# Kernel tuning notes

Hardware: AMD Instinct MI355X
Metric: run time of the kernel (lower is better)

Reference implementation:

```python
import jax, jax.numpy as jnp
import numpy as np

B = 65536      # batch
C = 1000       # num_classes
D = 256        # feat_dim


def _l2norm(x, eps=1e-12):
    # matches F.normalize(dim=1): v / max(||v||_2, eps)
    n = jnp.linalg.norm(x, axis=1, keepdims=True)
    return x / jnp.maximum(n, eps)


def setup_inputs() -> dict:
    key = jax.random.key(0)
    k1, k2, k3, k4, k5 = jax.random.split(key, 5)
    bound = 1.0 / np.sqrt(D)
    X = jax.random.normal(k1, (B, D), dtype=jnp.float32)
    labels = jax.random.randint(k2, (B,), 0, C)
    signatures = jax.random.uniform(k3, (C, D), dtype=jnp.float32, minval=-bound, maxval=bound)
    b_means = jax.random.uniform(k4, (1, D), dtype=jnp.float32, minval=-bound, maxval=bound)
    b_covs = jax.random.normal(k5, (D, D), dtype=jnp.float32)
    return {"X": X, "labels": labels, "signatures": signatures,
            "b_means": b_means, "b_covs": b_covs}


def reference(X, labels, signatures, b_means, b_covs):
    # SVD-based whitening of background covariance (tiny DxD)
    cov = b_covs @ b_covs.T
    U, eig, _ = jnp.linalg.svd(cov)
    DU = (eig ** -0.5)[:, None] * U.T              # diag(eig^-1/2) @ U^T, [D, D]
    xHat = _l2norm((X - b_means) @ DU.T)           # [B, D]
    sHat = _l2norm(signatures @ DU.T)              # [C, D]
    ACE_targets = xHat @ sHat.T                    # [B, C] cosine scores
    labels = labels.astype(jnp.int32)
    numerator = jnp.take_along_axis(ACE_targets, labels[:, None], axis=1)[:, 0]
    # denominator = exp(true) + sum(exp(others)) == sum over all classes
    loss = -jnp.mean(numerator - jax.nn.logsumexp(ACE_targets, axis=1))
    return (loss, ACE_targets)
```

## Files before the change

### kernel.cpp

```cpp
#include <hip/hip_runtime.h>
#include <hip/hip_bf16.h>
#include <math.h>

#define D_ 256
#define B_ 65536
#define C_ 1000

typedef _Float16 f16x8 __attribute__((ext_vector_type(8)));
typedef float f32x4 __attribute__((ext_vector_type(4)));

__global__ __launch_bounds__(256) void cov_kernel(const float* __restrict__ bc,
                                                  double* __restrict__ C64,
                                                  double* __restrict__ acc,
                                                  unsigned int* __restrict__ counter) {
  __shared__ float Ash[32][260];
  __shared__ float Bsh2[32][260];
  const int b = blockIdx.x, bi = b >> 3, bj = b & 7;
  const int e = threadIdx.x;
  if (b == 0 && e == 0) { *acc = 0.0; *counter = 0u; }
#pragma unroll
  for (int s = 0; s < 32; ++s) {
    int lin = s * 256 + e;
    int rr = lin >> 8, cc = lin & 255;
    Ash[rr][cc] = bc[(bi * 32 + rr) * 256 + cc];
    Bsh2[rr][cc] = bc[(bj * 32 + rr) * 256 + cc];
  }
  __syncthreads();
  const int tx = e & 15, ty = e >> 4;
  double a00 = 0, a01 = 0, a10 = 0, a11 = 0;
#pragma unroll 8
  for (int k = 0; k < 256; ++k) {
    double ar0 = (double)Ash[ty][k], ar1 = (double)Ash[ty + 16][k];
    double br0 = (double)Bsh2[tx][k], br1 = (double)Bsh2[tx + 16][k];
    a00 += ar0 * br0; a01 += ar0 * br1;
    a10 += ar1 * br0; a11 += ar1 * br1;
  }
  const int r0 = bi * 32, c0 = bj * 32;
  C64[(size_t)(r0 + ty) * D_ + c0 + tx] = a00;
  C64[(size_t)(r0 + ty) * D_ + c0 + tx + 16] = a01;
  C64[(size_t)(r0 + ty + 16) * D_ + c0 + tx] = a10;
  C64[(size_t)(r0 + ty + 16) * D_ + c0 + tx + 16] = a11;
}

__global__ __launch_bounds__(256, 1) void chol_panel(double* __restrict__ A, int p) {
  const int j0 = p * 64;
  const int r = threadIdx.x;
  __shared__ double raw[2][64];
  double pr[64];
  const bool act = (r >= j0);
  const bool inpanel = act && (r < j0 + 64);
  if (act) {
#pragma unroll
    for (int k = 0; k < 64; ++k) pr[k] = A[(size_t)r * D_ + j0 + k];
  }
  if (inpanel) raw[0][r - j0] = pr[0];
  __syncthreads();
#pragma unroll
  for (int j = 0; j < 64; ++j) {
    const int col = j0 + j;
    const double d2 = raw[j & 1][j];
    double rs = (double)rsqrtf((float)d2);
    rs = rs * (1.5 - 0.5 * d2 * rs * rs);
    rs = rs * (1.5 - 0.5 * d2 * rs * rs);
    if (r >= col) {
      const double lr_ = pr[j] * rs;
      pr[j] = lr_;
#pragma unroll
      for (int k = j + 1; k < 64; ++k) pr[k] -= lr_ * (raw[j & 1][k] * rs);
    }
    if (j < 63) {
      if (r > col && r < j0 + 64) raw[(j + 1) & 1][r - j0] = pr[j + 1];
    }
    __syncthreads();
  }
  if (act) {
    const int kmax = (r - j0 < 63) ? (r - j0) : 63;
#pragma unroll
    for (int k = 0; k < 64; ++k)
      if (k <= kmax) A[(size_t)r * D_ + j0 + k] = pr[k];
  }
}

__global__ __launch_bounds__(256) void chol_trail(double* __restrict__ A, int p) {
  const int j0 = p * 64;
  const int t0 = j0 + 64;
  int b = blockIdx.x, I = 0;
  while (b >= I + 1) { b -= I + 1; ++I; }
  const int J = b;
  const int r0 = t0 + I * 64, c0 = t0 + J * 64;
  __shared__ double LR[64][67];
  __shared__ double LC[64][67];
  const int tid = threadIdx.x;
  for (int e = tid; e < 64 * 64; e += 256) {
    int rr = e >> 6, cc = e & 63;
    LR[rr][cc] = A[(size_t)(r0 + rr) * D_ + j0 + cc];
    LC[rr][cc] = A[(size_t)(c0 + rr) * D_ + j0 + cc];
  }
  __syncthreads();
  const int tx = tid & 15, ty = tid >> 4;
  double acc[4][4];
#pragma unroll
  for (int i = 0; i < 4; ++i)
#pragma unroll
    for (int j = 0; j < 4; ++j) acc[i][j] = 0.0;
#pragma unroll 4
  for (int k = 0; k < 64; ++k) {
    double a_[4], b_[4];
#pragma unroll
    for (int i = 0; i < 4; ++i) a_[i] = LR[ty + 16 * i][k];
#pragma unroll
    for (int j = 0; j < 4; ++j) b_[j] = LC[tx + 16 * j][k];
#pragma unroll
    for (int i = 0; i < 4; ++i)
#pragma unroll
      for (int j = 0; j < 4; ++j) acc[i][j] += a_[i] * b_[j];
  }
#pragma unroll
  for (int i = 0; i < 4; ++i) {
    const int grow = r0 + ty + 16 * i;
#pragma unroll
    for (int j = 0; j < 4; ++j) {
      const int gcol = c0 + tx + 16 * j;
      A[(size_t)grow * D_ + gcol] -= acc[i][j];
    }
  }
}

__global__ __launch_bounds__(256) void inv_kernel(const double* __restrict__ L,
                                                  _Float16* __restrict__ WbP,
                                                  _Float16* __restrict__ WbT) {
  const int c = blockIdx.x;
  const int tid = threadIdx.x;
  __shared__ double w[D_];
  __shared__ double rdi[D_];
  __shared__ double rhs[32];
  __shared__ double Ldd[32][33];
  w[tid] = 0.0;
  rdi[tid] = 1.0 / L[(size_t)tid * D_ + tid];
  __syncthreads();
  const int q0 = c >> 5;
  for (int q = q0; q < 8; ++q) {
    const int i0 = q * 32;
    const int ii = tid >> 3, s = tid & 7;
    const int i = i0 + ii;
    double part = 0.0;
    for (int k = c + s; k < i0; k += 8) part += L[(size_t)i * D_ + k] * w[k];
    part += __shfl_xor(part, 1, 64);
    part += __shfl_xor(part, 2, 64);
    part += __shfl_xor(part, 4, 64);
    if (s == 0) rhs[ii] = ((i == c) ? 1.0 : 0.0) - part;
    for (int e = tid; e < 32 * 32; e += 256) {
      int rr = e >> 5, cc = e & 31;
      Ldd[rr][cc] = L[(size_t)(i0 + rr) * D_ + i0 + cc];
    }
    __syncthreads();
    if (tid < 32) {
      double x = rhs[tid];
      double v = 0.0;
      for (int j = 0; j < 32; ++j) {
        double xj = __shfl(x, j, 64);
        double wj = xj * rdi[i0 + j];
        if (tid == j) v = wj;
        if (tid > j) x -= Ldd[tid][j] * wj;
      }
      w[i0 + tid] = v;
    }
    __syncthreads();
  }
  _Float16 h = (_Float16)(float)w[tid];
  WbT[(size_t)c * D_ + tid] = h;
  {
    const int g = tid >> 4, lrr = tid & 15;
    const int ks = c >> 5, lqq = (c >> 3) & 3, jj = c & 7;
    WbP[(size_t)(g * 8 + ks) * 512 + (size_t)(lqq * 16 + lrr) * 8 + jj] = h;
  }
}

__global__ void sig_kernel(const float* __restrict__ S, const _Float16* __restrict__ WbT,
                           _Float16* __restrict__ sHatP) {
  int c = blockIdx.x, i = threadIdx.x;
  const int g = c >> 4, lr = c & 15;
  const int ks = i >> 5, lq = (i >> 3) & 3, jj = i & 7;
  const size_t off = (size_t)(g * 8 + ks) * 512 + (size_t)(lq * 16 + lr) * 8 + jj;
  if (c >= C_) { sHatP[off] = (_Float16)0.0f; return; }
  __shared__ float srow[D_];
  __shared__ float wred[4];
  srow[i] = S[c * D_ + i];
  __syncthreads();
  float t = 0.f;
  for (int k = 0; k < D_; ++k) t += (float)WbT[k * D_ + i] * srow[k];
  float ss = t * t;
#pragma unroll
  for (int d = 1; d < 64; d <<= 1) ss += __shfl_xor(ss, d, 64);
  if ((i & 63) == 0) wred[i >> 6] = ss;
  __syncthreads();
  float tot = wred[0] + wred[1] + wred[2] + wred[3];
  float rn = 1.0f / fmaxf(sqrtf(tot), 1e-12f);
  sHatP[off] = (_Float16)(t * rn);
}

__global__ __launch_bounds__(1024) void ace_kernel(const float* __restrict__ X,
                                                   const float* __restrict__ means,
                                                   const _Float16* __restrict__ WbP,
                                                   const _Float16* __restrict__ sHatP,
                                                   const int* __restrict__ labels,
                                                   float* __restrict__ out,
                                                   double* __restrict__ acc_loss,
                                                   unsigned int* __restrict__ counter) {
  __shared__ __align__(16) char ldsraw[131072];
  __shared__ float msh[D_];
  __shared__ float part[64];
  _Float16* const Wsh = (_Float16*)ldsraw;
  char* const xsC = ldsraw;
  _Float16* const Bsh = (_Float16*)ldsraw;
  float* const outACE = out + 1;

  const int tid = threadIdx.x;
  const int wid = tid >> 6, l = tid & 63, lr = l & 15, lq = l >> 4;
  const int rowbase = blockIdx.x * 256;
  const int wrow = rowbase + wid * 16;
  const int arow = wrow + lr;

  if (tid < 256) msh[tid] = means[tid];
#pragma unroll
  for (int s = 0; s < 8; ++s) {
    const int off = (wid * 8 + s) * 512;
    __builtin_amdgcn_global_load_lds(
        (const __attribute__((address_space(1))) unsigned int*)(WbP + off + l * 8),
        (__attribute__((address_space(3))) unsigned int*)(Wsh + off), 16, 0, 0);
  }
  __syncthreads();

  f16x8 af[8];
#pragma unroll
  for (int ks = 0; ks < 8; ++ks) {
    const float* xp = X + (size_t)arow * D_ + lq * 8 + ks * 32;
    const float4 x0 = *(const float4*)(xp);
    const float4 x1 = *(const float4*)(xp + 4);
    const int mb = lq * 8 + ks * 32;
    af[ks][0] = (_Float16)(x0.x - msh[mb + 0]);
    af[ks][1] = (_Float16)(x0.y - msh[mb + 1]);
    af[ks][2] = (_Float16)(x0.z - msh[mb + 2]);
    af[ks][3] = (_Float16)(x0.w - msh[mb + 3]);
    af[ks][4] = (_Float16)(x1.x - msh[mb + 4]);
    af[ks][5] = (_Float16)(x1.y - msh[mb + 5]);
    af[ks][6] = (_Float16)(x1.z - msh[mb + 6]);
    af[ks][7] = (_Float16)(x1.w - msh[mb + 7]);
  }
  f32x4 wacc[16];
#pragma unroll
  for (int u = 0; u < 16; ++u) wacc[u] = (f32x4){0.f, 0.f, 0.f, 0.f};
  {
    const _Float16* wb = Wsh + (size_t)l * 8;
#pragma unroll
    for (int ks = 0; ks < 8; ++ks) {
#pragma unroll
      for (int u = 0; u < 16; ++u) {
        f16x8 bf = *(const f16x8*)(wb + (u * 8 + ks) * 512);
        wacc[u] = __builtin_amdgcn_mfma_f32_16x16x32_f16(af[ks], bf, wacc[u], 0, 0, 0);
      }
    }
  }
  float ss[4] = {0.f, 0.f, 0.f, 0.f};
#pragma unroll
  for (int u = 0; u < 16; ++u)
#pragma unroll
    for (int j = 0; j < 4; ++j) ss[j] += wacc[u][j] * wacc[u][j];
#pragma unroll
  for (int d = 1; d < 16; d <<= 1) {
#pragma unroll
    for (int j = 0; j < 4; ++j) ss[j] += __shfl_xor(ss[j], d, 64);
  }
  float rx[4];
#pragma unroll
  for (int j = 0; j < 4; ++j) rx[j] = 1.0f / fmaxf(sqrtf(ss[j]), 1e-12f);

  __syncthreads();

#pragma unroll
  for (int u = 0; u < 16; ++u) {
#pragma unroll
    for (int j = 0; j < 4; ++j) {
      const int rowl = wid * 16 + lq * 4 + j;
      const int byte = (rowl * 512 + (u * 16 + lr) * 2) ^ ((rowl & 7) << 4);
      *(_Float16*)(xsC + byte) = (_Float16)wacc[u][j];
    }
  }
  __syncthreads();
  f16x8 a[8];
  {
    const int rowA = wid * 16 + lr;
#pragma unroll
    for (int ks = 0; ks < 8; ++ks) {
      const int byte = (rowA * 512 + ks * 64 + lq * 16) ^ ((rowA & 7) << 4);
      a[ks] = *(const f16x8*)(xsC + byte);
    }
  }
  __syncthreads();

  int lab[4]; float ssum[4], num[4];
#pragma unroll
  for (int j = 0; j < 4; ++j) {
    lab[j] = labels[wrow + lq * 4 + j];
    ssum[j] = 0.f; num[j] = 0.f;
  }

#define STAGE(bufi, chi) do {                                                        \
    const _Float16* _src = sHatP + (size_t)(chi) * 32768;                            \
    _Float16* _dst = Bsh + (size_t)(bufi) * 32768;                                   \
    _Pragma("unroll")                                                                \
    for (int _s = 0; _s < 4; ++_s) {                                                 \
      const int _off = wid * 2048 + _s * 512;                                        \
      __builtin_amdgcn_global_load_lds(                                              \
          (const __attribute__((address_space(1))) unsigned int*)(_src + _off + l * 8), \
          (__attribute__((address_space(3))) unsigned int*)(_dst + _off), 16, 0, 0); \
    } } while (0)

  float* const outrow = outACE + (size_t)(wrow + lq * 4) * C_;

  STAGE(0, 0);
  __syncthreads();
  int buf = 0;
  for (int ch = 0; ch < 8; ++ch) {
    if (ch < 7) {
      STAGE(buf ^ 1, ch + 1);
      __builtin_amdgcn_sched_barrier(0);
    }
    const _Float16* bb = Bsh + (size_t)buf * 32768 + (size_t)l * 8;
    f32x4 acc[8];
#pragma unroll
    for (int t = 0; t < 8; ++t) acc[t] = (f32x4){0.f, 0.f, 0.f, 0.f};
#pragma unroll
    for (int ks = 0; ks < 8; ++ks) {
#pragma unroll
      for (int t = 0; t < 8; ++t) {
        f16x8 bf = *(const f16x8*)(bb + (t * 8 + ks) * 512);
        acc[t] = __builtin_amdgcn_mfma_f32_16x16x32_f16(a[ks], bf, acc[t], 0, 0, 0);
      }
    }
#pragma unroll
    for (int t = 0; t < 8; ++t) {
      const int col = ch * 128 + t * 16 + lr;
      const bool valid = (col < C_);
#pragma unroll
      for (int j = 0; j < 4; ++j) {
        float v = acc[t][j] * rx[j];
        if (valid) outrow[(size_t)j * C_ + col] = v;
        ssum[j] += __expf(v - 1.0f);
        num[j] = (col == lab[j]) ? v : num[j];
      }
    }
    if (ch < 7) {
      __builtin_amdgcn_sched_barrier(0);
      asm volatile("s_waitcnt vmcnt(32)" ::: "memory");
      __builtin_amdgcn_s_barrier();
      __builtin_amdgcn_sched_barrier(0);
    }
    buf ^= 1;
  }
#undef STAGE

#pragma unroll
  for (int d2 = 1; d2 < 16; d2 <<= 1) {
#pragma unroll
    for (int j = 0; j < 4; ++j) {
      ssum[j] += __shfl_xor(ssum[j], d2, 64);
      num[j]  += __shfl_xor(num[j], d2, 64);
    }
  }
  if (lr == 0) {
    const float padcorr = 24.0f * __expf(-1.0f);
    float contrib = 0.f;
#pragma unroll
    for (int j = 0; j < 4; ++j)
      contrib += num[j] - (1.0f + __logf(ssum[j] - padcorr));
    part[wid * 4 + lq] = contrib;
  }
  __syncthreads();
  if (tid == 0) {
    float s = 0.f;
#pragma unroll
    for (int p2 = 0; p2 < 64; ++p2) s += part[p2];
    atomicAdd(acc_loss, (double)s);
    __threadfence();
    unsigned int old = atomicAdd(counter, 1u);
    if (old == (unsigned int)(gridDim.x - 1)) {
      __threadfence();
      double tot = atomicAdd(acc_loss, 0.0);
      out[0] = (float)(-tot / (double)B_);
    }
  }
}

extern "C" void kernel_launch(void* const* d_in, const int* in_sizes, int n_in,
                              void* d_out, int out_size, void* d_ws, size_t ws_size,
                              hipStream_t stream) {
  const float* X      = (const float*)d_in[0];
  const int*   labels = (const int*)d_in[1];
  const float* S      = (const float*)d_in[2];
  const float* means  = (const float*)d_in[3];
  const float* bc     = (const float*)d_in[4];
  float* out = (float*)d_out;

  char* w = (char*)d_ws;
  double*       acc   = (double*)(w + 0);
  unsigned int* cnt   = (unsigned int*)(w + 128);
  double*       C64   = (double*)(w + 256);
  _Float16*     WbP   = (_Float16*)(w + 524544);
  _Float16*     WbT   = (_Float16*)(w + 655616);
  _Float16*     sHatP = (_Float16*)(w + 786688);

  cov_kernel<<<64, 256, 0, stream>>>(bc, C64, acc, cnt);
  for (int p = 0; p < 4; ++p) {
    chol_panel<<<1, 256, 0, stream>>>(C64, p);
    int nt = 3 - p;
    if (nt > 0) chol_trail<<<nt * (nt + 1) / 2, 256, 0, stream>>>(C64, p);
  }
  inv_kernel<<<256, 256, 0, stream>>>(C64, WbP, WbT);
  sig_kernel<<<1024, 256, 0, stream>>>(S, WbT, sHatP);
  ace_kernel<<<256, 1024, 0, stream>>>(X, means, WbP, sHatP, labels, out, acc, cnt);
}
```

Measured before the change: 358.5 us.

## Factor Cholesky diagonal block in one wavefront via shuffles, then solve panel rows

The panel factorization is restructured. A single 64-lane wavefront now factors the 64x64 diagonal block using wave shuffles instead of shared-memory broadcasts with a block barrier per column. The rows below the diagonal block are then solved independently by a forward substitution against the stored factor, which needs only one barrier. This removes 64 block-wide synchronizations, at the cost of more shuffle traffic and serial work on one wave while the other lanes wait.

Result: slower. 1.080 ms (+201.2%).

```diff
diff --git a/kernel.cpp b/kernel.cpp
--- a/kernel.cpp
+++ b/kernel.cpp
@@ -44,40 +44,56 @@
 
 __global__ __launch_bounds__(256, 1) void chol_panel(double* __restrict__ A, int p) {
   const int j0 = p * 64;
-  const int r = threadIdx.x;
-  __shared__ double raw[2][64];
-  double pr[64];
-  const bool act = (r >= j0);
-  const bool inpanel = act && (r < j0 + 64);
-  if (act) {
+  const int tid = threadIdx.x;
+  __shared__ double Lp[64][65];
+  __shared__ double rsv[64];
+
+  const int rsub = j0 + tid;
+  const bool dosub = (tid >= 64) && (rsub < D_);
+  double x[64];
+  if (dosub) {
+#pragma unroll
+    for (int k = 0; k < 64; ++k) x[k] = A[(size_t)rsub * D_ + j0 + k];
+  }
+
+  if (tid < 64) {
+    const int r = j0 + tid;
+    double pr[64];
 #pragma unroll
     for (int k = 0; k < 64; ++k) pr[k] = A[(size_t)r * D_ + j0 + k];
-  }
-  if (inpanel) raw[0][r - j0] = pr[0];
-  __syncthreads();
-#pragma unroll
-  for (int j = 0; j < 64; ++j) {
-    const int col = j0 + j;
-    const double d2 = raw[j & 1][j];
-    double rs = (double)rsqrtf((float)d2);
-    rs = rs * (1.5 - 0.5 * d2 * rs * rs);
-    rs = rs * (1.5 - 0.5 * d2 * rs * rs);
-    if (r >= col) {
-      const double lr_ = pr[j] * rs;
-      pr[j] = lr_;
-#pragma unroll
-      for (int k = j + 1; k < 64; ++k) pr[k] -= lr_ * (raw[j & 1][k] * rs);
-    }
-    if (j < 63) {
-      if (r > col && r < j0 + 64) raw[(j + 1) & 1][r - j0] = pr[j + 1];
-    }
-    __syncthreads();
-  }
-  if (act) {
-    const int kmax = (r - j0 < 63) ? (r - j0) : 63;
+#pragma unroll
+    for (int j = 0; j < 64; ++j) {
+      const double d2 = __shfl(pr[j], j, 64);
+      double rs = (double)rsqrtf((float)d2);
+      rs = rs * (1.5 - 0.5 * d2 * rs * rs);
+      rs = rs * (1.5 - 0.5 * d2 * rs * rs);
+      const double lr = pr[j] * rs;
+      pr[j] = lr;
+      if (tid == j) rsv[j] = rs;
+#pragma unroll
+      for (int k = j + 1; k < 64; ++k) {
+        const double lkj = __shfl(lr, k, 64);
+        pr[k] -= lr * lkj;
+      }
+    }
+#pragma unroll
+    for (int k = 0; k < 64; ++k) Lp[tid][k] = pr[k];
 #pragma unroll
     for (int k = 0; k < 64; ++k)
-      if (k <= kmax) A[(size_t)r * D_ + j0 + k] = pr[k];
+      if (k <= tid) A[(size_t)r * D_ + j0 + k] = pr[k];
+  }
+  __syncthreads();
+
+  if (dosub) {
+#pragma unroll
+    for (int j = 0; j < 64; ++j) {
+      const double wj = x[j] * rsv[j];
+      x[j] = wj;
+#pragma unroll
+      for (int k = j + 1; k < 64; ++k) x[k] -= wj * Lp[k][j];
+    }
+#pragma unroll
+    for (int k = 0; k < 64; ++k) A[(size_t)rsub * D_ + j0 + k] = x[k];
   }
 }
 
```
